# Performance work log

Measured on AMD Instinct MI355X. Metric: run time of the kernel, lower is better.

Reference implementation:

```python
import jax, jax.numpy as jnp
import numpy as np

B, T, C, H = 2, 4096, 1024, 16
D = C // H
SEGMENTS = ((512, 1), (1024, 2), (2048, 4))  # (segment_length w, dilation r) per LongNet config


def setup_inputs() -> dict:
    key = jax.random.key(0)
    ks = jax.random.split(key, 12)
    s = 0.02
    return {
        "x": jax.random.normal(ks[0], (B, T, C), jnp.float32),
        # outer fused qkv projection (c_attn), stored as [in, out] so y = x @ W + b
        "c_attn_w": jax.random.normal(ks[1], (C, 3 * C), jnp.float32) * s,
        "c_attn_b": jnp.zeros((3 * C,), jnp.float32),
        # inner torchscale MultiheadAttention projections
        "q_w": jax.random.normal(ks[2], (C, C), jnp.float32) * s,
        "q_b": jnp.zeros((C,), jnp.float32),
        "k_w": jax.random.normal(ks[3], (C, C), jnp.float32) * s,
        "k_b": jnp.zeros((C,), jnp.float32),
        "v_w": jax.random.normal(ks[4], (C, C), jnp.float32) * s,
        "v_b": jnp.zeros((C,), jnp.float32),
        "o_w": jax.random.normal(ks[5], (C, C), jnp.float32) * s,
        "o_b": jnp.zeros((C,), jnp.float32),
    }


def _branch(q, k, v, w, r):
    """One dilated-attention branch: segment length w, dilation r.
    q,k,v: [B,H,T,D] (q pre-scaled). Heads use offset = head % r (LongNet).
    Returns (out_full [B,H,T,D], lse_full [B,H,T]) scattered back to full positions.
    """
    b, h_, t, d = q.shape
    n_seg, eff = t // w, w // r
    h = jnp.arange(h_)
    idx = (h % r)[:, None] + jnp.arange(eff)[None, :] * r            # [H, eff] within-segment indices
    pos = jnp.arange(n_seg)[None, :, None] * w + idx[:, None, :]     # [H, n_seg, eff] absolute positions
    hh = h[:, None, None]
    qg = q[:, hh, pos]                                               # [B,H,n_seg,eff,D]
    kg = k[:, hh, pos]
    vg = v[:, hh, pos]
    scores = jnp.einsum('bhsid,bhsjd->bhsij', qg, kg)
    causal = jnp.tril(jnp.ones((eff, eff), bool))                    # order preserved under strided subsampling
    scores = jnp.where(causal, scores, jnp.finfo(scores.dtype).min)
    m = scores.max(-1, keepdims=True)
    p = jnp.exp(scores - m)
    s = p.sum(-1, keepdims=True)
    o = jnp.einsum('bhsij,bhsjd->bhsid', p, vg) / s
    lse = m[..., 0] + jnp.log(s[..., 0])                             # [B,H,n_seg,eff]
    out_full = jnp.zeros((b, h_, t, d), q.dtype).at[:, hh, pos].set(o)
    lse_full = jnp.full((b, h_, t), -1e30, q.dtype).at[:, hh, pos].set(lse)
    return out_full, lse_full


def _forward(x, c_attn_w, c_attn_b, q_w, q_b, k_w, k_b, v_w, v_b, o_w, o_b):
    b, t, c = x.shape
    qkv = x @ c_attn_w + c_attn_b
    qx, kx, vx = jnp.split(qkv, 3, axis=-1)
    q = (qx @ q_w + q_b).reshape(b, t, H, D).transpose(0, 2, 1, 3) * (D ** -0.5)
    k = (kx @ k_w + k_b).reshape(b, t, H, D).transpose(0, 2, 1, 3)
    v = (vx @ v_w + v_b).reshape(b, t, H, D).transpose(0, 2, 1, 3)
    outs, lses = zip(*[_branch(q, k, v, w, r) for w, r in SEGMENTS])
    O = jnp.stack(outs)                                              # [S,B,H,T,D]
    L = jnp.stack(lses)                                              # [S,B,H,T]
    # LongNet combination: weight each branch by its softmax denominator (via lse)
    m = L.max(0)
    wts = jnp.exp(L - m)                                             # [S,B,H,T]
    y = (wts[..., None] * O).sum(0) / wts.sum(0)[..., None]          # [B,H,T,D]
    y = y.transpose(0, 2, 1, 3).reshape(b, t, c)
    return y @ o_w + o_b


def reference(x, c_attn_w, c_attn_b, q_w, q_b, k_w, k_b, v_w, v_b, o_w, o_b):
    return _forward(x, c_attn_w, c_attn_b, q_w, q_b, k_w, k_b, v_w, v_b, o_w, o_b)
```

## Files before the change

### kernel.cpp

```cpp
#include <hip/hip_runtime.h>
#include <hip/hip_bf16.h>

typedef __bf16 bf16x8 __attribute__((ext_vector_type(8)));
typedef float  f32x4  __attribute__((ext_vector_type(4)));

__device__ __forceinline__ unsigned short f2bf(float f) {
    union { float f; unsigned int u; } v; v.f = f;
    return (unsigned short)((v.u + 0x8000u) >> 16);
}
__device__ __forceinline__ float bf2f(unsigned short h) {
    union { unsigned int u; float f; } v; v.u = ((unsigned int)h) << 16;
    return v.f;
}

typedef __attribute__((address_space(3))) unsigned int lds_u32_t;
typedef const __attribute__((address_space(1))) unsigned int glb_u32_t;
__device__ __forceinline__ void gl_lds16(const void* g, void* l) {
    __builtin_amdgcn_global_load_lds((glb_u32_t*)g, (lds_u32_t*)l, 16, 0, 0);
}

__global__ void k_cast2(const float* __restrict__ a, unsigned short* __restrict__ oa,
                        const float* __restrict__ b, unsigned short* __restrict__ ob) {
    int blk = blockIdx.x;
    const float* in;
    unsigned short* out;
    int base;
    if (blk < 8192) { in = a; out = oa; base = blk * 1024; }
    else            { in = b; out = ob; base = (blk - 8192) * 1024; }
    int i = base + threadIdx.x * 4;
    float4 v = *reinterpret_cast<const float4*>(in + i);
    ushort4 o;
    o.x = f2bf(v.x); o.y = f2bf(v.y); o.z = f2bf(v.z); o.w = f2bf(v.w);
    *reinterpret_cast<ushort4*>(out + i) = o;
}

__global__ void k_transpose4(const float* __restrict__ s0, const float* __restrict__ s1,
                             const float* __restrict__ s2, const float* __restrict__ s3,
                             unsigned short* __restrict__ d0, unsigned short* __restrict__ d1,
                             unsigned short* __restrict__ d2, unsigned short* __restrict__ d3) {
    __shared__ float tile[32][33];
    int z = blockIdx.z;
    const float* in = (z == 0) ? s0 : (z == 1) ? s1 : (z == 2) ? s2 : s3;
    unsigned short* out = (z == 0) ? d0 : (z == 1) ? d1 : (z == 2) ? d2 : d3;
    int n0 = blockIdx.x * 32, k0 = blockIdx.y * 32;
    int tx = threadIdx.x, ty = threadIdx.y;
    #pragma unroll
    for (int i = 0; i < 4; ++i)
        tile[ty + i * 8][tx] = in[(size_t)(k0 + ty + i * 8) * 1024 + n0 + tx];
    __syncthreads();
    #pragma unroll
    for (int i = 0; i < 4; ++i)
        out[(size_t)(n0 + ty + i * 8) * 1024 + k0 + tx] = f2bf(tile[tx][ty + i * 8]);
}

__global__ __launch_bounds__(256) void k_gemm(
    const unsigned short* __restrict__ A, int lda,
    const unsigned short* __restrict__ Bt, int ldb,
    const float* __restrict__ bias,
    void* __restrict__ out,
    int M, int N, int K, int mode, float scale)
{
    __shared__ unsigned short As[8192];
    __shared__ unsigned short Bs[8192];
    int tid  = threadIdx.x;
    int lane = tid & 63, wv = tid >> 6;
    int quad = lane >> 4, l16 = lane & 15;

    int nwg = gridDim.x * gridDim.y;
    int lin = blockIdx.y * gridDim.x + blockIdx.x;
    int bx = blockIdx.x, by = blockIdx.y;
    if ((nwg & 7) == 0) {
        int swz = (lin & 7) * (nwg >> 3) + (lin >> 3);
        bx = swz % gridDim.x;
        by = swz / gridDim.x;
    }
    int bm = by * 128, bn = bx * 128;
    int wm = (wv >> 1) * 64,  wn = (wv & 1) * 64;

    f32x4 acc[4][4] = {};
    int srow = tid >> 2, scol = (tid & 3) * 8;

    for (int k0 = 0; k0 < K; k0 += 64) {
        #pragma unroll
        for (int kk = 0; kk < 2; ++kk)
            #pragma unroll
            for (int s = 0; s < 2; ++s) {
                int row = s * 64 + srow;
                gl_lds16(&A[(size_t)(bm + row) * lda + k0 + kk * 32 + scol], &As[kk * 4096 + (s * 256 + wv * 64) * 8]);
                gl_lds16(&Bt[(size_t)(bn + row) * ldb + k0 + kk * 32 + scol], &Bs[kk * 4096 + (s * 256 + wv * 64) * 8]);
            }
        __syncthreads();
        #pragma unroll
        for (int kk = 0; kk < 2; ++kk) {
            bf16x8 af[4], bfv[4];
            #pragma unroll
            for (int mi = 0; mi < 4; ++mi)
                af[mi] = *reinterpret_cast<const bf16x8*>(&As[kk * 4096 + (wm + mi * 16 + l16) * 32 + quad * 8]);
            #pragma unroll
            for (int ni = 0; ni < 4; ++ni)
                bfv[ni] = *reinterpret_cast<const bf16x8*>(&Bs[kk * 4096 + (wn + ni * 16 + l16) * 32 + quad * 8]);
            #pragma unroll
            for (int mi = 0; mi < 4; ++mi)
                #pragma unroll
                for (int ni = 0; ni < 4; ++ni)
                    acc[mi][ni] = __builtin_amdgcn_mfma_f32_16x16x32_bf16(bfv[ni], af[mi], acc[mi][ni], 0, 0, 0);
        }
        __syncthreads();
    }

    #pragma unroll
    for (int mi = 0; mi < 4; ++mi) {
        int row = bm + wm + mi * 16 + l16;
        #pragma unroll
        for (int ni = 0; ni < 4; ++ni) {
            int col0 = bn + wn + ni * 16 + quad * 4;
            float4 b4 = *reinterpret_cast<const float4*>(&bias[col0]);
            float v0 = (acc[mi][ni][0] + b4.x) * scale;
            float v1 = (acc[mi][ni][1] + b4.y) * scale;
            float v2 = (acc[mi][ni][2] + b4.z) * scale;
            float v3 = (acc[mi][ni][3] + b4.w) * scale;
            if (mode == 0) {
                ushort4 o4; o4.x = f2bf(v0); o4.y = f2bf(v1); o4.z = f2bf(v2); o4.w = f2bf(v3);
                *reinterpret_cast<ushort4*>(&reinterpret_cast<unsigned short*>(out)[(size_t)row * N + col0]) = o4;
            } else {
                float4 o4; o4.x = v0; o4.y = v1; o4.z = v2; o4.w = v3;
                *reinterpret_cast<float4*>(&reinterpret_cast<float*>(out)[(size_t)row * N + col0]) = o4;
            }
        }
    }
}

__global__ __launch_bounds__(256) void k_foldw(
    const unsigned short* __restrict__ wT3,
    const unsigned short* __restrict__ WcB,
    unsigned short* __restrict__ Weff)
{
    __shared__ unsigned short As[8192];
    __shared__ unsigned short Bs[8192];
    int z = blockIdx.z;
    const unsigned short* A  = wT3 + (size_t)z * 1024 * 1024;
    const unsigned short* Bt = WcB + z * 1024;
    unsigned short* out = Weff + (size_t)z * 1024 * 1024;
    float scale = (z == 0) ? 0.1803368801f : 1.f;

    int tid  = threadIdx.x;
    int lane = tid & 63, wv = tid >> 6;
    int quad = lane >> 4, l16 = lane & 15;
    int bm = blockIdx.y * 128, bn = blockIdx.x * 128;
    int wm = (wv >> 1) * 64,  wn = (wv & 1) * 64;

    f32x4 acc[4][4] = {};
    int srow = tid >> 2, scol = (tid & 3) * 8;

    for (int k0 = 0; k0 < 1024; k0 += 64) {
        #pragma unroll
        for (int kk = 0; kk < 2; ++kk)
            #pragma unroll
            for (int s = 0; s < 2; ++s) {
                int row = s * 64 + srow;
                gl_lds16(&A[(size_t)(bm + row) * 1024 + k0 + kk * 32 + scol], &As[kk * 4096 + (s * 256 + wv * 64) * 8]);
                gl_lds16(&Bt[(size_t)(bn + row) * 3072 + k0 + kk * 32 + scol], &Bs[kk * 4096 + (s * 256 + wv * 64) * 8]);
            }
        __syncthreads();
        #pragma unroll
        for (int kk = 0; kk < 2; ++kk) {
            bf16x8 af[4], bfv[4];
            #pragma unroll
            for (int mi = 0; mi < 4; ++mi)
                af[mi] = *reinterpret_cast<const bf16x8*>(&As[kk * 4096 + (wm + mi * 16 + l16) * 32 + quad * 8]);
            #pragma unroll
            for (int ni = 0; ni < 4; ++ni)
                bfv[ni] = *reinterpret_cast<const bf16x8*>(&Bs[kk * 4096 + (wn + ni * 16 + l16) * 32 + quad * 8]);
            #pragma unroll
            for (int mi = 0; mi < 4; ++mi)
                #pragma unroll
                for (int ni = 0; ni < 4; ++ni)
                    acc[mi][ni] = __builtin_amdgcn_mfma_f32_16x16x32_bf16(bfv[ni], af[mi], acc[mi][ni], 0, 0, 0);
        }
        __syncthreads();
    }

    #pragma unroll
    for (int mi = 0; mi < 4; ++mi) {
        int row = bm + wm + mi * 16 + l16;
        #pragma unroll
        for (int ni = 0; ni < 4; ++ni) {
            int col0 = bn + wn + ni * 16 + quad * 4;
            ushort4 o4;
            o4.x = f2bf(acc[mi][ni][0] * scale);
            o4.y = f2bf(acc[mi][ni][1] * scale);
            o4.z = f2bf(acc[mi][ni][2] * scale);
            o4.w = f2bf(acc[mi][ni][3] * scale);
            *reinterpret_cast<ushort4*>(&out[(size_t)row * 1024 + col0]) = o4;
        }
    }
}

__global__ __launch_bounds__(256) void k_foldb(
    const unsigned short* __restrict__ wT3, const float* __restrict__ bc,
    const float* __restrict__ qb, const float* __restrict__ kb,
    const float* __restrict__ vb, float* __restrict__ beff)
{
    int wv = threadIdx.x >> 6, lane = threadIdx.x & 63;
    int id = blockIdx.x * 4 + wv;
    int z = id >> 10, n = id & 1023;
    const unsigned short* row = wT3 + (size_t)z * 1024 * 1024 + (size_t)n * 1024;
    const float* bcz = bc + z * 1024;
    float s = 0.f;
    #pragma unroll
    for (int it = 0; it < 2; ++it) {
        int c0 = it * 512 + lane * 8;
        uint4 v = *reinterpret_cast<const uint4*>(&row[c0]);
        const unsigned short* pv = reinterpret_cast<const unsigned short*>(&v);
        float4 f0 = *reinterpret_cast<const float4*>(&bcz[c0]);
        float4 f1 = *reinterpret_cast<const float4*>(&bcz[c0 + 4]);
        s += f0.x * bf2f(pv[0]) + f0.y * bf2f(pv[1]) + f0.z * bf2f(pv[2]) + f0.w * bf2f(pv[3]);
        s += f1.x * bf2f(pv[4]) + f1.y * bf2f(pv[5]) + f1.z * bf2f(pv[6]) + f1.w * bf2f(pv[7]);
    }
    s += __shfl_xor(s, 1); s += __shfl_xor(s, 2); s += __shfl_xor(s, 4);
    s += __shfl_xor(s, 8); s += __shfl_xor(s, 16); s += __shfl_xor(s, 32);
    if (lane == 0) {
        const float* b2 = (z == 0) ? qb : (z == 1) ? kb : vb;
        float r = s + b2[n];
        if (z == 0) r *= 0.1803368801f;
        beff[id] = r;
    }
}

__global__ __launch_bounds__(256) void k_gemm3(
    const unsigned short* __restrict__ A,
    const unsigned short* __restrict__ Weff,
    const float* __restrict__ beff,
    unsigned short* __restrict__ Qg, unsigned short* __restrict__ Kg,
    unsigned short* __restrict__ Vtg)
{
    __shared__ unsigned short smem[16896];
    unsigned short* As = smem;
    unsigned short* Bs = smem + 8192;
    const int TS = 132;

    int tid  = threadIdx.x;
    int lane = tid & 63, wv = tid >> 6;
    int quad = lane >> 4, l16 = lane & 15;

    int nwg = gridDim.x * gridDim.y * gridDim.z;
    int lin = (blockIdx.z * gridDim.y + blockIdx.y) * gridDim.x + blockIdx.x;
    int swz = (lin & 7) * (nwg >> 3) + (lin >> 3);
    int bx  = swz & 7;
    int tmp = swz >> 3;
    int by  = tmp & 63;
    int z   = tmp >> 6;

    const unsigned short* Bt = Weff + (size_t)z * 1024 * 1024;
    const float* bias = beff + z * 1024;

    int bm = by * 128, bn = bx * 128;
    int wm = (wv >> 1) * 64,  wn = (wv & 1) * 64;

    f32x4 acc[4][4] = {};
    int srow = tid >> 2, scol = (tid & 3) * 8;

    for (int k0 = 0; k0 < 1024; k0 += 64) {
        #pragma unroll
        for (int kk = 0; kk < 2; ++kk)
            #pragma unroll
            for (int s = 0; s < 2; ++s) {
                int row = s * 64 + srow;
                gl_lds16(&A[(size_t)(bm + row) * 1024 + k0 + kk * 32 + scol], &As[kk * 4096 + (s * 256 + wv * 64) * 8]);
                gl_lds16(&Bt[(size_t)(bn + row) * 1024 + k0 + kk * 32 + scol], &Bs[kk * 4096 + (s * 256 + wv * 64) * 8]);
            }
        __syncthreads();
        #pragma unroll
        for (int kk = 0; kk < 2; ++kk) {
            bf16x8 af[4], bfv[4];
            #pragma unroll
            for (int mi = 0; mi < 4; ++mi)
                af[mi] = *reinterpret_cast<const bf16x8*>(&As[kk * 4096 + (wm + mi * 16 + l16) * 32 + quad * 8]);
            #pragma unroll
            for (int ni = 0; ni < 4; ++ni)
                bfv[ni] = *reinterpret_cast<const bf16x8*>(&Bs[kk * 4096 + (wn + ni * 16 + l16) * 32 + quad * 8]);
            if (z < 2) {
                #pragma unroll
                for (int mi = 0; mi < 4; ++mi)
                    #pragma unroll
                    for (int ni = 0; ni < 4; ++ni)
                        acc[mi][ni] = __builtin_amdgcn_mfma_f32_16x16x32_bf16(bfv[ni], af[mi], acc[mi][ni], 0, 0, 0);
            } else {
                #pragma unroll
                for (int mi = 0; mi < 4; ++mi)
                    #pragma unroll
                    for (int ni = 0; ni < 4; ++ni)
                        acc[mi][ni] = __builtin_amdgcn_mfma_f32_16x16x32_bf16(af[mi], bfv[ni], acc[mi][ni], 0, 0, 0);
            }
        }
        __syncthreads();
    }

    unsigned short* T = smem;
    int b  = bm >> 12, t0 = bm & 4095;
    int h0 = bn >> 6;
    int slot0 = t0 >> 9;
    int slot1 = 8 + (t0 >> 10);
    int slot2 = 12 + (t0 >> 11);

    if (z < 2) {
        unsigned short* dst = (z == 0) ? Qg : Kg;
        #pragma unroll
        for (int mi = 0; mi < 4; ++mi) {
            int tl = wm + mi * 16 + l16;
            #pragma unroll
            for (int ni = 0; ni < 4; ++ni) {
                int dl0 = wn + ni * 16 + quad * 4;
                float4 b4 = *reinterpret_cast<const float4*>(&bias[bn + dl0]);
                ushort4 o4;
                o4.x = f2bf(acc[mi][ni][0] + b4.x);
                o4.y = f2bf(acc[mi][ni][1] + b4.y);
                o4.z = f2bf(acc[mi][ni][2] + b4.z);
                o4.w = f2bf(acc[mi][ni][3] + b4.w);
                *reinterpret_cast<ushort4*>(&T[tl * TS + dl0]) = o4;
            }
        }
        __syncthreads();
        #pragma unroll
        for (int rep = 0; rep < 8; ++rep) {
            int c = rep * 256 + tid;
            int h = c >> 10, rr = c & 1023;
            int tl = rr >> 3, dseg = (rr & 7) * 8;
            int bh = b * 16 + h0 + h;
            size_t base = ((size_t)(slot0 * 32 + bh) * 512 + (t0 & 511) + tl) * 64;
            *reinterpret_cast<uint4*>(&dst[base + dseg]) =
                *reinterpret_cast<const uint4*>(&T[tl * TS + h * 64 + dseg]);
        }
        #pragma unroll
        for (int rep = 0; rep < 4; ++rep) {
            int c = rep * 256 + tid;
            int h = c >> 9, rr = c & 511;
            int i = rr >> 3, dseg = (rr & 7) * 8;
            int hh = h0 + h;
            int bh = b * 16 + hh;
            int tl = 2 * i + (hh & 1);
            size_t base = ((size_t)(slot1 * 32 + bh) * 512 + ((t0 & 1023) >> 1) + i) * 64;
            *reinterpret_cast<uint4*>(&dst[base + dseg]) =
                *reinterpret_cast<const uint4*>(&T[tl * TS + h * 64 + dseg]);
        }
        #pragma unroll
        for (int rep = 0; rep < 2; ++rep) {
            int c = rep * 256 + tid;
            int h = c >> 8, rr = c & 255;
            int i = rr >> 3, dseg = (rr & 7) * 8;
            int hh = h0 + h;
            int bh = b * 16 + hh;
            int tl = 4 * i + (hh & 3);
            size_t base = ((size_t)(slot2 * 32 + bh) * 512 + ((t0 & 2047) >> 2) + i) * 64;
            *reinterpret_cast<uint4*>(&dst[base + dseg]) =
                *reinterpret_cast<const uint4*>(&T[tl * TS + h * 64 + dseg]);
        }
    } else {
        #pragma unroll
        for (int ni = 0; ni < 4; ++ni) {
            int dl = wn + ni * 16 + l16;
            float bsv = bias[bn + dl];
            #pragma unroll
            for (int mi = 0; mi < 4; ++mi) {
                int tl0 = wm + mi * 16 + quad * 4;
                ushort4 o4;
                o4.x = f2bf(acc[mi][ni][0] + bsv);
                o4.y = f2bf(acc[mi][ni][1] + bsv);
                o4.z = f2bf(acc[mi][ni][2] + bsv);
                o4.w = f2bf(acc[mi][ni][3] + bsv);
                *reinterpret_cast<ushort4*>(&T[dl * TS + tl0]) = o4;
            }
        }
        __syncthreads();
        #pragma unroll
        for (int rep = 0; rep < 8; ++rep) {
            int c = rep * 256 + tid;
            int h = c >> 10, rr = c & 1023;
            int d = rr >> 4, seg = (rr & 15) * 8;
            int bh = b * 16 + h0 + h;
            size_t base = ((size_t)(slot0 * 32 + bh) * 64 + d) * 512 + (t0 & 511);
            *reinterpret_cast<uint4*>(&Vtg[base + seg]) =
                *reinterpret_cast<const uint4*>(&T[(h * 64 + d) * TS + seg]);
        }
        #pragma unroll
        for (int rep = 0; rep < 4; ++rep) {
            int c = rep * 256 + tid;
            int h = c >> 9, rr = c & 511;
            int d = rr >> 3, seg = rr & 7;
            int hh = h0 + h;
            int bh = b * 16 + hh;
            int p = hh & 1;
            const unsigned short* srw = &T[(h * 64 + d) * TS];
            unsigned short buf[8];
            #pragma unroll
            for (int j = 0; j < 8; ++j) buf[j] = srw[p + 2 * (seg * 8 + j)];
            size_t base = ((size_t)(slot1 * 32 + bh) * 64 + d) * 512 + ((t0 & 1023) >> 1);
            *reinterpret_cast<uint4*>(&Vtg[base + seg * 8]) = *reinterpret_cast<const uint4*>(buf);
        }
        #pragma unroll
        for (int rep = 0; rep < 2; ++rep) {
            int c = rep * 256 + tid;
            int h = c >> 8, rr = c & 255;
            int d = rr >> 2, seg = rr & 3;
            int hh = h0 + h;
            int bh = b * 16 + hh;
            int p = hh & 3;
            const unsigned short* srw = &T[(h * 64 + d) * TS];
            unsigned short buf[8];
            #pragma unroll
            for (int j = 0; j < 8; ++j) buf[j] = srw[p + 4 * (seg * 8 + j)];
            size_t base = ((size_t)(slot2 * 32 + bh) * 64 + d) * 512 + ((t0 & 2047) >> 2);
            *reinterpret_cast<uint4*>(&Vtg[base + seg * 8]) = *reinterpret_cast<const uint4*>(buf);
        }
    }
}

__global__ __launch_bounds__(256, 3) void k_attn(
    const unsigned short* __restrict__ Qg,
    const unsigned short* __restrict__ Kg,
    const unsigned short* __restrict__ Vtg,
    unsigned short* __restrict__ Og,
    float* __restrict__ Lg)
{
    __shared__ unsigned short Ks[2][64 * 72];
    __shared__ unsigned short Vs[2][64 * 72];

    int tid  = threadIdx.x;
    int lane = tid & 63, wv = tid >> 6;
    int quad = lane >> 4, l16 = lane & 15;
    int q8   = quad << 3;
    int pq = blockIdx.x, ys = blockIdx.y, bh = blockIdx.z;
    int jt_end = 2 * (3 - pq) + 1;
    size_t sb = (size_t)(ys * 32 + bh) * (512 * 64);
    const unsigned short* qp = Qg + sb;
    const unsigned short* kp = Kg + sb;
    const unsigned short* vp = Vtg + sb;
    unsigned short* op = Og + sb;
    float* lp = Lg + (size_t)(ys * 32 + bh) * 512;

    int rw[2] = { pq * 128 + wv * 32, (3 - pq) * 128 + wv * 32 };

    int srow = tid >> 3, sc8 = (tid & 7) * 8;
    int prow = ((srow >> 2) & 1) * 16 + ((srow >> 3) & 3) * 4 + (srow & 3);
    uint4 kr[2], vr[2];
    {
        #pragma unroll
        for (int s = 0; s < 2; ++s) {
            int row = s * 32 + srow;
            kr[s] = *reinterpret_cast<const uint4*>(&kp[(size_t)row * 64 + sc8]);
            vr[s] = *reinterpret_cast<const uint4*>(&vp[(size_t)row * 512 + sc8]);
        }
    }

    bf16x8 qf[2][2][2];
    #pragma unroll
    for (int qi = 0; qi < 2; ++qi)
        #pragma unroll
        for (int m16 = 0; m16 < 2; ++m16)
            #pragma unroll
            for (int kk = 0; kk < 2; ++kk)
                qf[qi][m16][kk] = *reinterpret_cast<const bf16x8*>(
                    &qp[(size_t)(rw[qi] + m16 * 16 + l16) * 64 + kk * 32 + quad * 8]);

    f32x4 acc[2][2][4] = {};
    float l4[2][2] = {};

    for (int jt = 0; jt <= jt_end; ++jt) {
        unsigned short* Kb = &Ks[jt & 1][0];
        unsigned short* Vb = &Vs[jt & 1][0];
        #pragma unroll
        for (int s = 0; s < 2; ++s) {
            *reinterpret_cast<uint4*>(&Kb[(s * 32 + prow) * 72 + sc8]) = kr[s];
            *reinterpret_cast<uint4*>(&Vb[(s * 32 + srow) * 72 + sc8]) = vr[s];
        }
        if (jt < jt_end) {
            #pragma unroll
            for (int s = 0; s < 2; ++s) {
                int row = s * 32 + srow;
                kr[s] = *reinterpret_cast<const uint4*>(&kp[(size_t)((jt + 1) * 64 + row) * 64 + sc8]);
                vr[s] = *reinterpret_cast<const uint4*>(&vp[(size_t)row * 512 + (jt + 1) * 64 + sc8]);
            }
        }
        __syncthreads();

        #pragma unroll
        for (int qi = 0; qi < 2; ++qi) {
            #pragma unroll
            for (int m16 = 0; m16 < 2; ++m16) {
                int rowbase = rw[qi] + m16 * 16;
                if (jt * 64 > rowbase + 15) continue;

                f32x4 sacc[4];
                __builtin_amdgcn_s_setprio(1);
                #pragma unroll
                for (int nt = 0; nt < 4; ++nt) {
                    bf16x8 b0 = *reinterpret_cast<const bf16x8*>(&Kb[(nt * 16 + l16) * 72 + quad * 8]);
                    bf16x8 b1 = *reinterpret_cast<const bf16x8*>(&Kb[(nt * 16 + l16) * 72 + 32 + quad * 8]);
                    f32x4 s4 = {};
                    s4 = __builtin_amdgcn_mfma_f32_16x16x32_bf16(b0, qf[qi][m16][0], s4, 0, 0, 0);
                    s4 = __builtin_amdgcn_mfma_f32_16x16x32_bf16(b1, qf[qi][m16][1], s4, 0, 0, 0);
                    sacc[nt] = s4;
                }
                __builtin_amdgcn_s_setprio(0);

                if (jt * 64 + 63 > rowbase) {
                    int qrow = rowbase + l16;
                    #pragma unroll
                    for (int nt = 0; nt < 4; ++nt)
                        #pragma unroll
                        for (int ri = 0; ri < 4; ++ri) {
                            int kj = jt * 64 + (nt >> 1) * 32 + (nt & 1) * 4 + q8 + ri;
                            if (kj > qrow) sacc[nt][ri] = -1e30f;
                        }
                }
                float ls = 0.f;
                #pragma unroll
                for (int nt = 0; nt < 4; ++nt)
                    #pragma unroll
                    for (int ri = 0; ri < 4; ++ri) {
                        float p = __builtin_amdgcn_exp2f(sacc[nt][ri]);
                        sacc[nt][ri] = p;
                        ls += p;
                    }
                l4[qi][m16] += ls;

                union { unsigned int u[4]; bf16x8 v; } p0u, p1u;
                asm("v_cvt_pk_bf16_f32 %0, %1, %2" : "=v"(p0u.u[0]) : "v"(sacc[0][0]), "v"(sacc[0][1]));
                asm("v_cvt_pk_bf16_f32 %0, %1, %2" : "=v"(p0u.u[1]) : "v"(sacc[0][2]), "v"(sacc[0][3]));
                asm("v_cvt_pk_bf16_f32 %0, %1, %2" : "=v"(p0u.u[2]) : "v"(sacc[1][0]), "v"(sacc[1][1]));
                asm("v_cvt_pk_bf16_f32 %0, %1, %2" : "=v"(p0u.u[3]) : "v"(sacc[1][2]), "v"(sacc[1][3]));
                asm("v_cvt_pk_bf16_f32 %0, %1, %2" : "=v"(p1u.u[0]) : "v"(sacc[2][0]), "v"(sacc[2][1]));
                asm("v_cvt_pk_bf16_f32 %0, %1, %2" : "=v"(p1u.u[1]) : "v"(sacc[2][2]), "v"(sacc[2][3]));
                asm("v_cvt_pk_bf16_f32 %0, %1, %2" : "=v"(p1u.u[2]) : "v"(sacc[3][0]), "v"(sacc[3][1]));
                asm("v_cvt_pk_bf16_f32 %0, %1, %2" : "=v"(p1u.u[3]) : "v"(sacc[3][2]), "v"(sacc[3][3]));

                __builtin_amdgcn_s_setprio(1);
                #pragma unroll
                for (int dt = 0; dt < 4; ++dt) {
                    bf16x8 v0 = *reinterpret_cast<const bf16x8*>(&Vb[(dt * 16 + l16) * 72 + quad * 8]);
                    bf16x8 v1 = *reinterpret_cast<const bf16x8*>(&Vb[(dt * 16 + l16) * 72 + 32 + quad * 8]);
                    f32x4 a4 = acc[qi][m16][dt];
                    a4 = __builtin_amdgcn_mfma_f32_16x16x32_bf16(p0u.v, v0, a4, 0, 0, 0);
                    a4 = __builtin_amdgcn_mfma_f32_16x16x32_bf16(p1u.v, v1, a4, 0, 0, 0);
                    acc[qi][m16][dt] = a4;
                }
                __builtin_amdgcn_s_setprio(0);
            }
        }
    }

    #pragma unroll
    for (int qi = 0; qi < 2; ++qi)
        #pragma unroll
        for (int m16 = 0; m16 < 2; ++m16) {
            int rowb = rw[qi] + m16 * 16;
            float L = l4[qi][m16];
            L += __shfl_xor(L, 16);
            L += __shfl_xor(L, 32);
            float inv[4];
            #pragma unroll
            for (int ri = 0; ri < 4; ++ri)
                inv[ri] = 1.f / __shfl(L, quad * 4 + ri);
            #pragma unroll
            for (int dt = 0; dt < 4; ++dt)
                #pragma unroll
                for (int ri = 0; ri < 4; ++ri) {
                    int row = rowb + quad * 4 + ri;
                    op[(size_t)row * 64 + dt * 16 + l16] = f2bf(acc[qi][m16][dt][ri] * inv[ri]);
                }
            if (lane < 16)
                lp[rowb + l16] = __logf(L);
        }
}

__global__ void k_combine(const unsigned short* __restrict__ Og,
                          const float* __restrict__ Lg,
                          unsigned short* __restrict__ yb)
{
    int g   = blockIdx.x * blockDim.x + threadIdx.x;
    int row = g >> 3;
    int d0  = (g & 7) * 8;
    int bh = row >> 12, t = row & 4095;
    int b = bh >> 4, h = bh & 15;

    int slot0 = t >> 9,         idx0 = t & 511;
    int slot1 = 8 + (t >> 10),  idx1 = (t & 1023) >> 1;
    int slot2 = 12 + (t >> 11), idx2 = (t & 2047) >> 2;
    size_t r0 = (size_t)(slot0 * 32 + bh) * 512 + idx0;
    size_t r1 = (size_t)(slot1 * 32 + bh) * 512 + idx1;
    size_t r2 = (size_t)(slot2 * 32 + bh) * 512 + idx2;
    bool c1 = ((t ^ h) & 1) == 0;
    bool c2 = ((t ^ h) & 3) == 0;

    float L0 = Lg[r0];
    float L1 = c1 ? Lg[r1] : -1e30f;
    float L2 = c2 ? Lg[r2] : -1e30f;
    float m  = fmaxf(L0, fmaxf(L1, L2));
    float w0 = __expf(L0 - m), w1 = __expf(L1 - m), w2 = __expf(L2 - m);
    float inv = 1.f / (w0 + w1 + w2);

    uint4 v0 = *reinterpret_cast<const uint4*>(&Og[r0 * 64 + d0]);
    uint4 v1 = *reinterpret_cast<const uint4*>(&Og[r1 * 64 + d0]);
    uint4 v2 = *reinterpret_cast<const uint4*>(&Og[r2 * 64 + d0]);
    const unsigned short* p0 = reinterpret_cast<const unsigned short*>(&v0);
    const unsigned short* p1 = reinterpret_cast<const unsigned short*>(&v1);
    const unsigned short* p2 = reinterpret_cast<const unsigned short*>(&v2);
    unsigned short o[8];
    #pragma unroll
    for (int u = 0; u < 8; ++u)
        o[u] = f2bf((w0 * bf2f(p0[u]) + w1 * bf2f(p1[u]) + w2 * bf2f(p2[u])) * inv);
    size_t yidx = (((size_t)b * 4096 + t) * 1024) + (size_t)h * 64 + d0;
    *reinterpret_cast<uint4*>(&yb[yidx]) = *reinterpret_cast<const uint4*>(o);
}

extern "C" void kernel_launch(void* const* d_in, const int* in_sizes, int n_in,
                              void* d_out, int out_size, void* d_ws, size_t ws_size,
                              hipStream_t stream)
{
    const float* x        = (const float*)d_in[0];
    const float* c_attn_w = (const float*)d_in[1];
    const float* c_attn_b = (const float*)d_in[2];
    const float* q_w      = (const float*)d_in[3];
    const float* q_b      = (const float*)d_in[4];
    const float* k_w      = (const float*)d_in[5];
    const float* k_b      = (const float*)d_in[6];
    const float* v_w      = (const float*)d_in[7];
    const float* v_b      = (const float*)d_in[8];
    const float* o_w      = (const float*)d_in[9];
    const float* o_b      = (const float*)d_in[10];

    char* ws = (char*)d_ws;
    size_t off = 0;
    auto alloc = [&](size_t bytes) -> char* {
        char* p = ws + off; off += (bytes + 255) & ~(size_t)255; return p;
    };
    const size_t GSZ = 14ull * 32 * 512 * 64;
    unsigned short* xb    = (unsigned short*)alloc(8192ull * 1024 * 2);
    unsigned short* WcB   = (unsigned short*)alloc(1024ull * 3072 * 2);
    unsigned short* wqT   = (unsigned short*)alloc(1024ull * 1024 * 2);
    unsigned short* wkT   = (unsigned short*)alloc(1024ull * 1024 * 2);
    unsigned short* wvT   = (unsigned short*)alloc(1024ull * 1024 * 2);
    unsigned short* woT   = (unsigned short*)alloc(1024ull * 1024 * 2);
    unsigned short* Weff  = (unsigned short*)alloc(3ull * 1024 * 1024 * 2);
    float*          beff  = (float*)alloc(3ull * 1024 * 4);
    unsigned short* Qg    = (unsigned short*)alloc(GSZ * 2);
    unsigned short* Kg    = (unsigned short*)alloc(GSZ * 2);
    unsigned short* Vtg   = (unsigned short*)alloc(GSZ * 2);
    unsigned short* Og    = (unsigned short*)alloc(GSZ * 2);
    float*          Lg    = (float*)alloc(14ull * 32 * 512 * 4);
    unsigned short* yb    = xb;
    (void)wkT; (void)wvT;

    k_cast2<<<8192 + 3072, 256, 0, stream>>>(x, xb, c_attn_w, WcB);
    k_transpose4<<<dim3(32, 32, 4), dim3(32, 8), 0, stream>>>(q_w, k_w, v_w, o_w, wqT, wkT, wvT, woT);
    k_foldw<<<dim3(8, 8, 3), 256, 0, stream>>>(wqT, WcB, Weff);
    k_foldb<<<768, 256, 0, stream>>>(wqT, c_attn_b, q_b, k_b, v_b, beff);
    k_gemm3<<<dim3(8, 64, 3), 256, 0, stream>>>(xb, Weff, beff, Qg, Kg, Vtg);
    k_attn<<<dim3(2, 14, 32), 256, 0, stream>>>(Qg, Kg, Vtg, Og, Lg);
    k_combine<<<4096, 256, 0, stream>>>(Og, Lg, yb);
    k_gemm<<<dim3(8, 64), 256, 0, stream>>>(yb, 1024, woT, 1024, o_b, d_out, 8192, 1024, 1024, 2, 1.f);
}
```

Measured before the change: 315.2 us.

## Double-buffer A tiles in LDS and load B fragments directly from global

In the three GEMM kernels the B operand no longer goes through LDS. Each wave reads its B fragments straight from global memory into registers. The A tile is now double-buffered, so the next tile's async global-to-LDS load is issued after the barrier and overlaps the current MFMA work, and the per-iteration trailing barrier is removed. The intent is to halve LDS traffic and hide load latency; the cost is uncoalesced, redundant global reads of B (each wave-pair rereads the same rows) and more live registers.

```diff
diff --git a/kernel.cpp b/kernel.cpp
--- a/kernel.cpp
+++ b/kernel.cpp
@@ -60,8 +60,7 @@
     void* __restrict__ out,
     int M, int N, int K, int mode, float scale)
 {
-    __shared__ unsigned short As[8192];
-    __shared__ unsigned short Bs[8192];
+    __shared__ unsigned short As[16384];
     int tid  = threadIdx.x;
     int lane = tid & 63, wv = tid >> 6;
     int quad = lane >> 4, l16 = lane & 15;
@@ -79,33 +78,50 @@
 
     f32x4 acc[4][4] = {};
     int srow = tid >> 2, scol = (tid & 3) * 8;
-
-    for (int k0 = 0; k0 < K; k0 += 64) {
+    const unsigned short* brow = &Bt[(size_t)(bn + wn + l16) * ldb + quad * 8];
+
+    #pragma unroll
+    for (int kk = 0; kk < 2; ++kk)
+        #pragma unroll
+        for (int s = 0; s < 2; ++s) {
+            int row = s * 64 + srow;
+            gl_lds16(&A[(size_t)(bm + row) * lda + kk * 32 + scol], &As[kk * 4096 + (s * 256 + wv * 64) * 8]);
+        }
+
+    int nk = K >> 6;
+    for (int i = 0; i < nk; ++i) {
+        int k0 = i << 6;
+        int cur = (i & 1) * 8192;
+        bf16x8 bfv[2][4];
         #pragma unroll
         for (int kk = 0; kk < 2; ++kk)
             #pragma unroll
-            for (int s = 0; s < 2; ++s) {
-                int row = s * 64 + srow;
-                gl_lds16(&A[(size_t)(bm + row) * lda + k0 + kk * 32 + scol], &As[kk * 4096 + (s * 256 + wv * 64) * 8]);
-                gl_lds16(&Bt[(size_t)(bn + row) * ldb + k0 + kk * 32 + scol], &Bs[kk * 4096 + (s * 256 + wv * 64) * 8]);
-            }
+            for (int ni = 0; ni < 4; ++ni)
+                bfv[kk][ni] = *reinterpret_cast<const bf16x8*>(&brow[(size_t)ni * 16 * ldb + k0 + kk * 32]);
         __syncthreads();
+        if (i + 1 < nk) {
+            int nxt = ((i + 1) & 1) * 8192;
+            #pragma unroll
+            for (int kk = 0; kk < 2; ++kk)
+                #pragma unroll
+                for (int s = 0; s < 2; ++s) {
+                    int row = s * 64 + srow;
+                    gl_lds16(&A[(size_t)(bm + row) * lda + k0 + 64 + kk * 32 + scol],
+                             &As[nxt + kk * 4096 + (s * 256 + wv * 64) * 8]);
+                }
+        }
         #pragma unroll
         for (int kk = 0; kk < 2; ++kk) {
-            bf16x8 af[4], bfv[4];
+            bf16x8 af[4];
             #pragma unroll
             for (int mi = 0; mi < 4; ++mi)
-                af[mi] = *reinterpret_cast<const bf16x8*>(&As[kk * 4096 + (wm + mi * 16 + l16) * 32 + quad * 8]);
-            #pragma unroll
-            for (int ni = 0; ni < 4; ++ni)
-                bfv[ni] = *reinterpret_cast<const bf16x8*>(&Bs[kk * 4096 + (wn + ni * 16 + l16) * 32 + quad * 8]);
+                af[mi] = *reinterpret_cast<const bf16x8*>(&As[cur + kk * 4096 + (wm + mi * 16 + l16) * 32 + quad * 8]);
             #pragma unroll
             for (int mi = 0; mi < 4; ++mi)
                 #pragma unroll
                 for (int ni = 0; ni < 4; ++ni)
-                    acc[mi][ni] = __builtin_amdgcn_mfma_f32_16x16x32_bf16(bfv[ni], af[mi], acc[mi][ni], 0, 0, 0);
-        }
-        __syncthreads();
+                    acc[mi][ni] = __builtin_amdgcn_mfma_f32_16x16x32_bf16(bfv[kk][ni], af[mi], acc[mi][ni], 0, 0, 0);
+        }
     }
 
     #pragma unroll
@@ -135,8 +151,7 @@
     const unsigned short* __restrict__ WcB,
     unsigned short* __restrict__ Weff)
 {
-    __shared__ unsigned short As[8192];
-    __shared__ unsigned short Bs[8192];
+    __shared__ unsigned short As[16384];
     int z = blockIdx.z;
     const unsigned short* A  = wT3 + (size_t)z * 1024 * 1024;
     const unsigned short* Bt = WcB + z * 1024;
@@ -151,33 +166,49 @@
 
     f32x4 acc[4][4] = {};
     int srow = tid >> 2, scol = (tid & 3) * 8;
-
-    for (int k0 = 0; k0 < 1024; k0 += 64) {
+    const unsigned short* brow = &Bt[(size_t)(bn + wn + l16) * 3072 + quad * 8];
+
+    #pragma unroll
+    for (int kk = 0; kk < 2; ++kk)
+        #pragma unroll
+        for (int s = 0; s < 2; ++s) {
+            int row = s * 64 + srow;
+            gl_lds16(&A[(size_t)(bm + row) * 1024 + kk * 32 + scol], &As[kk * 4096 + (s * 256 + wv * 64) * 8]);
+        }
+
+    for (int i = 0; i < 16; ++i) {
+        int k0 = i << 6;
+        int cur = (i & 1) * 8192;
+        bf16x8 bfv[2][4];
         #pragma unroll
         for (int kk = 0; kk < 2; ++kk)
             #pragma unroll
-            for (int s = 0; s < 2; ++s) {
-                int row = s * 64 + srow;
-                gl_lds16(&A[(size_t)(bm + row) * 1024 + k0 + kk * 32 + scol], &As[kk * 4096 + (s * 256 + wv * 64) * 8]);
-                gl_lds16(&Bt[(size_t)(bn + row) * 3072 + k0 + kk * 32 + scol], &Bs[kk * 4096 + (s * 256 + wv * 64) * 8]);
-            }
+            for (int ni = 0; ni < 4; ++ni)
+                bfv[kk][ni] = *reinterpret_cast<const bf16x8*>(&brow[(size_t)ni * 16 * 3072 + k0 + kk * 32]);
         __syncthreads();
+        if (i + 1 < 16) {
+            int nxt = ((i + 1) & 1) * 8192;
+            #pragma unroll
+            for (int kk = 0; kk < 2; ++kk)
+                #pragma unroll
+                for (int s = 0; s < 2; ++s) {
+                    int row = s * 64 + srow;
+                    gl_lds16(&A[(size_t)(bm + row) * 1024 + k0 + 64 + kk * 32 + scol],
+                             &As[nxt + kk * 4096 + (s * 256 + wv * 64) * 8]);
+                }
+        }
         #pragma unroll
         for (int kk = 0; kk < 2; ++kk) {
-            bf16x8 af[4], bfv[4];
+            bf16x8 af[4];
             #pragma unroll
             for (int mi = 0; mi < 4; ++mi)
-                af[mi] = *reinterpret_cast<const bf16x8*>(&As[kk * 4096 + (wm + mi * 16 + l16) * 32 + quad * 8]);
-            #pragma unroll
-            for (int ni = 0; ni < 4; ++ni)
-                bfv[ni] = *reinterpret_cast<const bf16x8*>(&Bs[kk * 4096 + (wn + ni * 16 + l16) * 32 + quad * 8]);
+                af[mi] = *reinterpret_cast<const bf16x8*>(&As[cur + kk * 4096 + (wm + mi * 16 + l16) * 32 + quad * 8]);
             #pragma unroll
             for (int mi = 0; mi < 4; ++mi)
                 #pragma unroll
                 for (int ni = 0; ni < 4; ++ni)
-                    acc[mi][ni] = __builtin_amdgcn_mfma_f32_16x16x32_bf16(bfv[ni], af[mi], acc[mi][ni], 0, 0, 0);
-        }
-        __syncthreads();
+                    acc[mi][ni] = __builtin_amdgcn_mfma_f32_16x16x32_bf16(bfv[kk][ni], af[mi], acc[mi][ni], 0, 0, 0);
+        }
     }
 
     #pragma unroll
@@ -236,7 +267,6 @@
 {
     __shared__ unsigned short smem[16896];
     unsigned short* As = smem;
-    unsigned short* Bs = smem + 8192;
     const int TS = 132;
 
     int tid  = threadIdx.x;
@@ -259,42 +289,59 @@
 
     f32x4 acc[4][4] = {};
     int srow = tid >> 2, scol = (tid & 3) * 8;
-
-    for (int k0 = 0; k0 < 1024; k0 += 64) {
+    const unsigned short* brow = &Bt[(size_t)(bn + wn + l16) * 1024 + quad * 8];
+
+    #pragma unroll
+    for (int kk = 0; kk < 2; ++kk)
+        #pragma unroll
+        for (int s = 0; s < 2; ++s) {
+            int row = s * 64 + srow;
+            gl_lds16(&A[(size_t)(bm + row) * 1024 + kk * 32 + scol], &As[kk * 4096 + (s * 256 + wv * 64) * 8]);
+        }
+
+    for (int i = 0; i < 16; ++i) {
+        int k0 = i << 6;
+        int cur = (i & 1) * 8192;
+        bf16x8 bfv[2][4];
         #pragma unroll
         for (int kk = 0; kk < 2; ++kk)
             #pragma unroll
-            for (int s = 0; s < 2; ++s) {
-                int row = s * 64 + srow;
-                gl_lds16(&A[(size_t)(bm + row) * 1024 + k0 + kk * 32 + scol], &As[kk * 4096 + (s * 256 + wv * 64) * 8]);
-                gl_lds16(&Bt[(size_t)(bn + row) * 1024 + k0 + kk * 32 + scol], &Bs[kk * 4096 + (s * 256 + wv * 64) * 8]);
-            }
+            for (int ni = 0; ni < 4; ++ni)
+                bfv[kk][ni] = *reinterpret_cast<const bf16x8*>(&brow[(size_t)ni * 16 * 1024 + k0 + kk * 32]);
         __syncthreads();
+        if (i + 1 < 16) {
+            int nxt = ((i + 1) & 1) * 8192;
+            #pragma unroll
+            for (int kk = 0; kk < 2; ++kk)
+                #pragma unroll
+                for (int s = 0; s < 2; ++s) {
+                    int row = s * 64 + srow;
+                    gl_lds16(&A[(size_t)(bm + row) * 1024 + k0 + 64 + kk * 32 + scol],
+                             &As[nxt + kk * 4096 + (s * 256 + wv * 64) * 8]);
+                }
+        }
         #pragma unroll
         for (int kk = 0; kk < 2; ++kk) {
-            bf16x8 af[4], bfv[4];
+            bf16x8 af[4];
             #pragma unroll
             for (int mi = 0; mi < 4; ++mi)
-                af[mi] = *reinterpret_cast<const bf16x8*>(&As[kk * 4096 + (wm + mi * 16 + l16) * 32 + quad * 8]);
-            #pragma unroll
-            for (int ni = 0; ni < 4; ++ni)
-                bfv[ni] = *reinterpret_cast<const bf16x8*>(&Bs[kk * 4096 + (wn + ni * 16 + l16) * 32 + quad * 8]);
+                af[mi] = *reinterpret_cast<const bf16x8*>(&As[cur + kk * 4096 + (wm + mi * 16 + l16) * 32 + quad * 8]);
             if (z < 2) {
                 #pragma unroll
                 for (int mi = 0; mi < 4; ++mi)
                     #pragma unroll
                     for (int ni = 0; ni < 4; ++ni)
-                        acc[mi][ni] = __builtin_amdgcn_mfma_f32_16x16x32_bf16(bfv[ni], af[mi], acc[mi][ni], 0, 0, 0);
+                        acc[mi][ni] = __builtin_amdgcn_mfma_f32_16x16x32_bf16(bfv[kk][ni], af[mi], acc[mi][ni], 0, 0, 0);
             } else {
                 #pragma unroll
                 for (int mi = 0; mi < 4; ++mi)
                     #pragma unroll
                     for (int ni = 0; ni < 4; ++ni)
-                        acc[mi][ni] = __builtin_amdgcn_mfma_f32_16x16x32_bf16(af[mi], bfv[ni], acc[mi][ni], 0, 0, 0);
+                        acc[mi][ni] = __builtin_amdgcn_mfma_f32_16x16x32_bf16(af[mi], bfv[kk][ni], acc[mi][ni], 0, 0, 0);
             }
         }
-        __syncthreads();
-    }
+    }
+    __syncthreads();
 
     unsigned short* T = smem;
     int b  = bm >> 12, t0 = bm & 4095;
```

New measurement: 374.0 us. 1.19x slower.
